# Optimization experiments

Measured on AMD Instinct MI355X. Metric: run time of the kernel, lower is better.

Reference implementation:

```python
import jax, jax.numpy as jnp
import numpy as np


def _l2norm(x, eps=1e-6):
    return x / jnp.sqrt(jnp.sum(x * x, axis=-1, keepdims=True) + eps)


def setup_inputs() -> dict:
    key = jax.random.key(0)
    k1, k2, k3, k4 = jax.random.split(key, 4)
    b, h, L, dk, dv = 2, 8, 4096, 128, 128
    q = jax.random.normal(k1, (b, h, L, dk), jnp.float32)
    k = jax.random.normal(k2, (b, h, L, dk), jnp.float32)
    v = jax.random.normal(k3, (b, h, L, dv), jnp.float32)
    beta = jax.random.uniform(k4, (b, h, L), jnp.float32)  # sigmoid(b_proj) in module -> (0,1)
    return {"q": q, "k": k, "v": v, "beta": beta, "chunk_size": 32}


def _delta_rule_chunkwise(q, k, v, beta, chunk_size):
    b, h, L, dk = q.shape
    dv = v.shape[-1]
    c = chunk_size
    pad = (-L) % c
    if pad:
        q = jnp.pad(q, ((0, 0), (0, 0), (0, pad), (0, 0)))
        k = jnp.pad(k, ((0, 0), (0, 0), (0, pad), (0, 0)))
        v = jnp.pad(v, ((0, 0), (0, 0), (0, pad), (0, 0)))
        beta = jnp.pad(beta, ((0, 0), (0, 0), (0, pad)))
    Lp = L + pad
    n = Lp // c

    q = _l2norm(q)
    k = _l2norm(k)
    v = v * beta[..., None]
    kb = k * beta[..., None]

    # (b,h,n,c,d)
    resh = lambda t: t.reshape(b, h, n, c, t.shape[-1])
    q, k, v, kb = resh(q), resh(k), resh(v), resh(kb)

    tri = jnp.triu(jnp.ones((c, c), bool), 0)        # upper incl diag
    tri_s = jnp.triu(jnp.ones((c, c), bool), 1)      # strict upper

    # forward substitution: inv = (I + strictly-lower(k_beta k^T))^{-1}-style recurrence
    inv = -jnp.einsum('bhncd,bhned->bhnce', kb, k)
    inv = jnp.where(tri, 0.0, inv)
    for i in range(1, c):  # fixed small chunk_size loop (c=32)
        upd = jnp.einsum('bhnk,bhnkj->bhnj', inv[..., i, :], inv[..., :, :i])
        inv = inv.at[..., i, :i].add(upd)
    inv = inv + jnp.eye(c, dtype=inv.dtype)

    u = inv @ v    # (b,h,n,c,dv)
    w = inv @ kb   # (b,h,n,c,dk)

    # chunk-recurrent state scan over the n blocks
    qs = jnp.moveaxis(q, 2, 0)
    ks = jnp.moveaxis(k, 2, 0)
    us = jnp.moveaxis(u, 2, 0)
    ws = jnp.moveaxis(w, 2, 0)
    S0 = jnp.zeros((b, h, dk, dv), q.dtype)

    def step(S, blk):
        q_i, k_i, u_i, w_i = blk
        attn = jnp.einsum('bhcd,bhed->bhce', q_i, k_i)
        attn = jnp.where(tri_s, 0.0, attn)                       # causal within chunk
        u_i = u_i - jnp.einsum('bhcd,bhde->bhce', w_i, S)
        o_i = jnp.einsum('bhcd,bhde->bhce', q_i, S) + jnp.einsum('bhce,bhed->bhcd', attn, u_i)
        S = S + jnp.einsum('bhcd,bhce->bhde', k_i, u_i)
        return S, o_i

    S, out = jax.lax.scan(step, S0, (qs, ks, us, ws))
    out = jnp.moveaxis(out, 0, 2).reshape(b, h, Lp, dv)[:, :, :L]
    return out, S


def reference(q, k, v, beta, chunk_size):
    return _delta_rule_chunkwise(q, k, v, beta, int(chunk_size))
```

## Files before the change

### kernel.cpp

```cpp
#include <hip/hip_runtime.h>
#include <cstddef>

#define BH   16
#define LSEQ 4096
#define DK   128
#define DV   128
#define C    32
#define NCH  128
#define DVB  16
#define NDVB 8
#define PP   136
#define PC   40
#define PS   136
#define AP   33

#define RECSZ 22528
#define OQ    0
#define OWH   4096
#define OWL   8192
#define OKTH  12288
#define OKTL  16384
#define OATH  20480
#define OATL  21504

typedef __attribute__((ext_vector_type(4))) float f32x4;
typedef __attribute__((ext_vector_type(8))) short short8;
typedef __attribute__((ext_vector_type(4))) short s16x4;

__device__ inline unsigned split_bf16(float x) {
    unsigned u = __builtin_bit_cast(unsigned, x);
    unsigned r = u + 0x7fffu + ((u >> 16) & 1u);
    unsigned h = r >> 16;
    float hf = __builtin_bit_cast(float, r & 0xffff0000u);
    float res = x - hf;
    unsigned u2 = __builtin_bit_cast(unsigned, res);
    unsigned r2 = u2 + 0x7fffu + ((u2 >> 16) & 1u);
    return (h << 16) | (r2 >> 16);
}
__device__ inline short hi_bf16(float x) {
    unsigned u = __builtin_bit_cast(unsigned, x);
    return (short)((u + 0x7fffu + ((u >> 16) & 1u)) >> 16);
}
__device__ inline short trunc_bf16(float x) {
    return (short)(__builtin_bit_cast(unsigned, x) >> 16);
}

__device__ inline short8 fld(const short* P, int row0, int pitch, int k0, int lane) {
    return *(const short8*)(P + (row0 + (lane & 15)) * pitch + k0 + ((lane >> 4) << 3));
}
__device__ inline short8 fldz128(const short* P, int row0, int ks, int lane) {
    int row = row0 + (lane & 15);
    int c = ks * 4 + (lane >> 4);
    return *(const short8*)(P + row * 128 + ((c ^ (row & 7)) << 3));
}
__device__ inline short8 fldz32(const short* P, int row0, int lane) {
    int row = row0 + (lane & 15);
    int c = lane >> 4;
    return *(const short8*)(P + row * 32 + ((c ^ (row & 3)) << 3));
}
__device__ inline f32x4 mf(short8 a, short8 b, f32x4 c) {
    return __builtin_amdgcn_mfma_f32_16x16x32_bf16(a, b, c, 0, 0, 0);
}
__device__ inline void build_ifrags(int lane, short8& Iev, short8& Iod) {
    int n = lane & 15, q = lane >> 4;
#pragma unroll
    for (int j = 0; j < 8; ++j) {
        Iev[j] = (q * 8 + j == n)      ? (short)0x3F80 : (short)0;
        Iod[j] = (q * 8 + j == n + 16) ? (short)0x3F80 : (short)0;
    }
}
__device__ inline void store8_z128(short* Pg, int row, int col0, s16x4 v) {
    int c = col0 >> 3;
    *(s16x4*)(Pg + row * 128 + ((c ^ (row & 7)) << 3) + (col0 & 7)) = v;
}
__device__ inline void store8_z32(short* Pg, int row, int col0, s16x4 v) {
    int c = col0 >> 3;
    *(s16x4*)(Pg + row * 32 + ((c ^ (row & 3)) << 3) + (col0 & 7)) = v;
}
__device__ inline void dma1k(const short* g, short* l, int lane) {
    __builtin_amdgcn_global_load_lds(
        (const __attribute__((address_space(1))) unsigned int*)(g + lane * 8),
        (__attribute__((address_space(3))) unsigned int*)l, 16, 0, 0);
}

__global__ __launch_bounds__(512) void k_prep(const float* __restrict__ Q,
                                              const float* __restrict__ K,
                                              const float* __restrict__ V,
                                              const float* __restrict__ Beta,
                                              short* __restrict__ RECg,
                                              float* __restrict__ Uws) {
    __shared__ short knh[C * PP], knl[C * PP], vh[C * PP], vl[C * PP], qh[C * PP];
    __shared__ short knTh[DK * PC], knTl[DK * PC], vTh[DK * PC], vTl[DK * PC];
    __shared__ short Th[C * PC], Tl[C * PC];
    __shared__ float A[C * AP];
    __shared__ float sbeta[C];

    const int t = threadIdx.x, lane = t & 63, wv = t >> 6;
    const int quad = (t >> 4) & 3, l15 = t & 15;
    const int g = blockIdx.x;
    const size_t base = (size_t)g * (C * DK);
    short* rec = RECg + (size_t)g * RECSZ;
    short8 Iev, Iod;
    build_ifrags(lane, Iev, Iod);

    if (t < C) sbeta[t] = Beta[(size_t)(g >> 7) * LSEQ + (size_t)(g & 127) * C + t];

    {
        const int sr = t >> 4, sc = (t & 15) * 8;
        f32x4 kk[2], vv[2], qq[2];
#pragma unroll
        for (int g4 = 0; g4 < 2; ++g4) {
            kk[g4] = *(const f32x4*)(K + base + 8 * t + 4 * g4);
            vv[g4] = *(const f32x4*)(V + base + 8 * t + 4 * g4);
            qq[g4] = *(const f32x4*)(Q + base + 8 * t + 4 * g4);
        }
        float ssk = 0.f, ssq = 0.f;
#pragma unroll
        for (int g4 = 0; g4 < 2; ++g4) {
#pragma unroll
            for (int e = 0; e < 4; ++e) {
                ssk += kk[g4][e] * kk[g4][e];
                ssq += qq[g4][e] * qq[g4][e];
            }
        }
        ssk += __shfl_xor(ssk, 1); ssk += __shfl_xor(ssk, 2);
        ssk += __shfl_xor(ssk, 4); ssk += __shfl_xor(ssk, 8);
        ssq += __shfl_xor(ssq, 1); ssq += __shfl_xor(ssq, 2);
        ssq += __shfl_xor(ssq, 4); ssq += __shfl_xor(ssq, 8);
        const float rk = rsqrtf(ssk + 1e-6f), rq = rsqrtf(ssq + 1e-6f);
        short8 h8, l8, q8;
#pragma unroll
        for (int e = 0; e < 8; ++e) {
            unsigned p = split_bf16(kk[e >> 2][e & 3] * rk);
            h8[e] = (short)(p >> 16); l8[e] = (short)(p & 0xffffu);
        }
        *(short8*)(knh + sr * PP + sc) = h8;
        *(short8*)(knl + sr * PP + sc) = l8;
#pragma unroll
        for (int e = 0; e < 8; ++e) {
            unsigned p = split_bf16(vv[e >> 2][e & 3]);
            h8[e] = (short)(p >> 16); l8[e] = (short)(p & 0xffffu);
        }
        *(short8*)(vh + sr * PP + sc) = h8;
        *(short8*)(vl + sr * PP + sc) = l8;
#pragma unroll
        for (int e = 0; e < 8; ++e) q8[e] = hi_bf16(qq[e >> 2][e & 3] * rq);
        *(short8*)(qh + sr * PP + sc) = q8;
        int c = sc >> 3;
        *(short8*)(rec + OQ + sr * 128 + ((c ^ (sr & 7)) << 3)) = q8;
    }
    __syncthreads();

    if (wv < 3) {
        const int a0 = (wv == 0) ? 0 : 16;
        const int b0 = (wv == 2) ? 16 : 0;
        f32x4 acc = {0.f, 0.f, 0.f, 0.f};
#pragma unroll
        for (int ks = 0; ks < 4; ++ks) {
            short8 ah = fld(knh, a0, PP, ks * 32, lane);
            short8 al = fld(knl, a0, PP, ks * 32, lane);
            short8 bh_ = fld(knh, b0, PP, ks * 32, lane);
            short8 bl_ = fld(knl, b0, PP, ks * 32, lane);
            acc = mf(ah, bh_, mf(ah, bl_, mf(al, bh_, acc)));
        }
#pragma unroll
        for (int r = 0; r < 4; ++r) {
            int row = a0 + quad * 4 + r, col = b0 + l15;
            A[row * AP + col] = (row > col) ? -sbeta[row] * acc[r] : 0.f;
        }
        f32x4 at = {0.f, 0.f, 0.f, 0.f};
#pragma unroll
        for (int ks = 0; ks < 4; ++ks) {
            short8 kh_ = fld(knh, b0, PP, ks * 32, lane);
            short8 kl_ = fld(knl, b0, PP, ks * 32, lane);
            short8 qf = fld(qh, a0, PP, ks * 32, lane);
            at = mf(kh_, qf, mf(kl_, qf, at));
        }
        s16x4 h4, l4;
#pragma unroll
        for (int r = 0; r < 4; ++r) {
            int cj = b0 + quad * 4 + r, ci = a0 + l15;
            float v = (cj <= ci) ? at[r] : 0.f;
            unsigned p = split_bf16(v);
            h4[r] = (short)(p >> 16); l4[r] = (short)(p & 0xffffu);
        }
        store8_z32(rec + OATH, a0 + l15, b0 + quad * 4, h4);
        store8_z32(rec + OATL, a0 + l15, b0 + quad * 4, l4);
    } else if (wv == 3) {
#pragma unroll
        for (int r = 0; r < 4; ++r) A[l15 * AP + 16 + quad * 4 + r] = 0.f;
        s16x4 z = {0, 0, 0, 0};
        store8_z32(rec + OATH, l15, 16 + quad * 4, z);
        store8_z32(rec + OATL, l15, 16 + quad * 4, z);
    }
    __syncthreads();

    auto tplane1 = [&](const short* src, short* dst, short* gdst, int c0) {
#pragma unroll
        for (int ks = 0; ks < 4; ++ks) {
            short8 fr = fld(src, c0, PP, ks * 32, lane);
            f32x4 z = {0.f, 0.f, 0.f, 0.f};
            f32x4 cA = mf(fr, Iev, z);
            f32x4 cB = mf(fr, Iod, z);
            s16x4 sA, sB;
#pragma unroll
            for (int r = 0; r < 4; ++r) { sA[r] = trunc_bf16(cA[r]); sB[r] = trunc_bf16(cB[r]); }
            *(s16x4*)(dst + (ks * 32 + l15) * PC + c0 + quad * 4) = sA;
            *(s16x4*)(dst + (ks * 32 + 16 + l15) * PC + c0 + quad * 4) = sB;
            if (gdst) {
                store8_z32(gdst, ks * 32 + l15, c0 + quad * 4, sA);
                store8_z32(gdst, ks * 32 + 16 + l15, c0 + quad * 4, sB);
            }
        }
    };
    if (wv == 0)      tplane1(knh, knTh, rec + OKTH, 0);
    else if (wv == 4) tplane1(knh, knTh, rec + OKTH, 16);
    else if (wv == 1) tplane1(knl, knTl, rec + OKTL, 0);
    else if (wv == 5) tplane1(knl, knTl, rec + OKTL, 16);
    else if (wv == 2) tplane1(vh, vTh, nullptr, 0);
    else if (wv == 6) tplane1(vh, vTh, nullptr, 16);
    else if (wv == 7) { tplane1(vl, vTl, nullptr, 0); tplane1(vl, vTl, nullptr, 16); }
    else if (lane < C) {
        const int j = lane;
        for (int i = 1; i < C; ++i) {
            float upd = 0.f;
            for (int kk2 = 1; kk2 < i; ++kk2) upd += A[i * AP + kk2] * A[kk2 * AP + j];
            if (j < i) A[i * AP + j] += upd;
        }
    }
    __syncthreads();

    if (t < 256) {
        int tr = t >> 3, tc = (t & 7) * 4;
        s16x4 h4, l4;
#pragma unroll
        for (int e = 0; e < 4; ++e) {
            int j = tc + e;
            float val = ((tr == j) ? 1.f : (tr > j ? A[tr * AP + j] : 0.f)) * sbeta[j];
            unsigned p = split_bf16(val);
            h4[e] = (short)(p >> 16); l4[e] = (short)(p & 0xffffu);
        }
        *(s16x4*)(Th + tr * PC + tc) = h4;
        *(s16x4*)(Tl + tr * PC + tc) = l4;
    }
    __syncthreads();

    {
        const int ci0 = (wv & 1) * 16;
        short8 bTh = fld(Th, ci0, PC, 0, lane);
        short8 bTl = fld(Tl, ci0, PC, 0, lane);
        if (wv < 4) {
            const int tb = (wv >> 1) * 4;
#pragma unroll
            for (int k = 0; k < 4; ++k) {
                int tt = tb + k;
                short8 ah = fld(vTh, tt * 16, PC, 0, lane);
                short8 al = fld(vTl, tt * 16, PC, 0, lane);
                f32x4 z = {0.f, 0.f, 0.f, 0.f};
                f32x4 acc = mf(ah, bTh, mf(ah, bTl, mf(al, bTh, z)));
                *(f32x4*)(Uws + (size_t)g * 4096 + (size_t)(ci0 + l15) * DK + tt * 16 + quad * 4) = acc;
            }
        } else {
            const int tb = ((wv - 4) >> 1) * 4;
#pragma unroll
            for (int k = 0; k < 4; ++k) {
                int tt = tb + k;
                short8 ah = fld(knTh, tt * 16, PC, 0, lane);
                short8 al = fld(knTl, tt * 16, PC, 0, lane);
                f32x4 z = {0.f, 0.f, 0.f, 0.f};
                f32x4 acc = mf(ah, bTh, mf(ah, bTl, mf(al, bTh, z)));
                s16x4 h4, l4;
#pragma unroll
                for (int r = 0; r < 4; ++r) {
                    unsigned p = split_bf16(acc[r]);
                    h4[r] = (short)(p >> 16); l4[r] = (short)(p & 0xffffu);
                }
                store8_z128(rec + OWH, ci0 + l15, tt * 16 + quad * 4, h4);
                store8_z128(rec + OWL, ci0 + l15, tt * 16 + quad * 4, l4);
            }
        }
    }
}

__global__ __launch_bounds__(512, 1) void k_scan(const short* __restrict__ RECg,
                                                 const float* __restrict__ Uws,
                                                 float* __restrict__ Out,
                                                 float* __restrict__ Sout) {
    __shared__ __attribute__((aligned(16))) short bALL[2][RECSZ];
    __shared__ short STh[DVB * PS], STl[DVB * PS];
    __shared__ short uTh[DVB * PC], uTl[DVB * PC];

    const int t = threadIdx.x, lane = t & 63, wv = t >> 6;
    const int quad = (t >> 4) & 3, l15 = t & 15;
    const int db = blockIdx.x >> 4, bhi = blockIdx.x & 15;
    const int vcol = db * DVB;
    const int r0 = (wv & 1) * 16;
    const int dk0 = wv * 16;
    const size_t gb = (size_t)bhi * NCH;

    f32x4 accS = {0.f, 0.f, 0.f, 0.f};
    float pu[4] = {0.f, 0.f, 0.f, 0.f};

    auto dma_chunk = [&](int cc, int s) {
        if (wv < 2) return;
        const short* src = RECg + (size_t)(gb + cc) * RECSZ;
        short* dst = bALL[s];
#pragma unroll
        for (int k = 0; k < 8; ++k) {
            int q = (wv - 2) + 6 * k;
            if (q < 44) dma1k(src + q * 512, dst + q * 512, lane);
        }
    };
    auto pref_u = [&](int cc) {
        if (wv < 2) {
            const size_t ub = (gb + cc) * 4096;
#pragma unroll
            for (int r = 0; r < 4; ++r)
                pu[r] = Uws[ub + (size_t)(r0 + quad * 4 + r) * DK + vcol + l15];
        }
    };

    for (int e = t; e < DVB * PS; e += 512) { STh[e] = 0; STl[e] = 0; }
    dma_chunk(0, 0);
    pref_u(0);
    __syncthreads();

    for (int cid = 0; cid < NCH; ++cid) {
        const int cur = cid & 1;
        const short* pC = bALL[cur];
        f32x4 oc = {0.f, 0.f, 0.f, 0.f};

        short8 kth = fldz32(pC + OKTH, dk0, lane);
        short8 ktl = fldz32(pC + OKTL, dk0, lane);
        short8 bah = {}, bal = {};

        if (wv >= 2) {
            if (cid + 1 < NCH) dma_chunk(cid + 1, cur ^ 1);
        } else {
            float p0 = pu[0], p1 = pu[1], p2 = pu[2], p3 = pu[3];
            if (cid + 1 < NCH) pref_u(cid + 1);

            f32x4 u0 = {-p0, -p1, -p2, -p3};
            f32x4 u1 = {0.f, 0.f, 0.f, 0.f}, u2 = {0.f, 0.f, 0.f, 0.f};
            f32x4 o1 = {0.f, 0.f, 0.f, 0.f};
#pragma unroll
            for (int ks = 0; ks < 4; ++ks) {
                short8 wh_ = fldz128(pC + OWH, r0, ks, lane);
                short8 wl_ = fldz128(pC + OWL, r0, ks, lane);
                short8 sh_ = fld(STh, 0, PS, ks * 32, lane);
                short8 sl_ = fld(STl, 0, PS, ks * 32, lane);
                short8 qf = fldz128(pC + OQ, r0, ks, lane);
                u0 = mf(wh_, sh_, u0);
                u1 = mf(wh_, sl_, u1);
                u2 = mf(wl_, sh_, u2);
                oc = mf(sh_, qf, oc);
                o1 = mf(sl_, qf, o1);
            }
            oc += o1;
            f32x4 us = u0 + u1 + u2;
            s16x4 h4, l4;
#pragma unroll
            for (int r = 0; r < 4; ++r) {
                unsigned p = split_bf16(-us[r]);
                h4[r] = (short)(p >> 16); l4[r] = (short)(p & 0xffffu);
            }
            *(s16x4*)(uTh + l15 * PC + r0 + quad * 4) = h4;
            *(s16x4*)(uTl + l15 * PC + r0 + quad * 4) = l4;
            bah = fldz32(pC + OATH, r0, lane);
            bal = fldz32(pC + OATL, r0, lane);
        }
        __syncthreads();

        short8 buh = fld(uTh, 0, PC, 0, lane);
        short8 bul = fld(uTl, 0, PC, 0, lane);
        if (wv < 2) {
            oc = mf(buh, bah, mf(buh, bal, mf(bul, bah, oc)));
            const size_t ob = ((size_t)bhi * LSEQ + (size_t)cid * C) * DK;
            *(f32x4*)(Out + ob + (size_t)(r0 + l15) * DK + vcol + quad * 4) = oc;
        }
        {
            f32x4 z = {0.f, 0.f, 0.f, 0.f};
            f32x4 tband = mf(kth, bul, mf(ktl, buh, z));
            accS = mf(kth, buh, accS);
            accS += tband;
            s16x4 h4, l4;
#pragma unroll
            for (int r = 0; r < 4; ++r) {
                unsigned p = split_bf16(accS[r]);
                h4[r] = (short)(p >> 16); l4[r] = (short)(p & 0xffffu);
            }
            *(s16x4*)(STh + l15 * PS + dk0 + quad * 4) = h4;
            *(s16x4*)(STl + l15 * PS + dk0 + quad * 4) = l4;
        }
        __syncthreads();
    }

#pragma unroll
    for (int r = 0; r < 4; ++r)
        Sout[(size_t)bhi * DK * DV + (size_t)(dk0 + quad * 4 + r) * DV + vcol + l15] = accS[r];
}

extern "C" void kernel_launch(void* const* d_in, const int* in_sizes, int n_in,
                              void* d_out, int out_size, void* d_ws, size_t ws_size,
                              hipStream_t stream) {
    const float* Q    = (const float*)d_in[0];
    const float* K    = (const float*)d_in[1];
    const float* V    = (const float*)d_in[2];
    const float* Beta = (const float*)d_in[3];

    float* Out  = (float*)d_out;
    float* Sout = Out + (size_t)BH * LSEQ * DV;

    short* RECg = (short*)d_ws;
    float* Uws  = (float*)(RECg + (size_t)BH * NCH * RECSZ);

    hipLaunchKernelGGL(k_prep, dim3(BH * NCH), dim3(512), 0, stream,
                       Q, K, V, Beta, RECg, Uws);
    hipLaunchKernelGGL(k_scan, dim3(BH * NDVB), dim3(512), 0, stream,
                       RECg, Uws, Out, Sout);
}
```

Baseline: 339.9 us.

## Compute u redundantly per wave to drop one block barrier per chunk

Every wave now computes the full 32-row u correction (S·W) itself and writes it to a private LDS slot. This removes the barrier that previously separated the u computation in two waves from the state update in all eight waves. The output computation moves to waves 2 and 3, and the DMA prefetch moves to the other six waves. The chunk loop is unrolled by two with separate named buffers and register prefetch arrays, so buffer indexing is static. The cost is redundant MFMA work, more LDS reads of W and S per wave, and higher register pressure.

Result: slower. 430.4 us (+26.6%).

```diff
diff --git a/kernel.cpp b/kernel.cpp
--- a/kernel.cpp
+++ b/kernel.cpp
@@ -286,77 +286,85 @@
                                                  const float* __restrict__ Uws,
                                                  float* __restrict__ Out,
                                                  float* __restrict__ Sout) {
-    __shared__ __attribute__((aligned(16))) short bALL[2][RECSZ];
+    __shared__ __attribute__((aligned(16))) short bufA[RECSZ];
+    __shared__ __attribute__((aligned(16))) short bufB[RECSZ];
     __shared__ short STh[DVB * PS], STl[DVB * PS];
-    __shared__ short uTh[DVB * PC], uTl[DVB * PC];
+    __shared__ short uSh[8][16 * PC], uSl[8][16 * PC];
 
     const int t = threadIdx.x, lane = t & 63, wv = t >> 6;
     const int quad = (t >> 4) & 3, l15 = t & 15;
     const int db = blockIdx.x >> 4, bhi = blockIdx.x & 15;
     const int vcol = db * DVB;
-    const int r0 = (wv & 1) * 16;
+    const int r02 = (wv & 1) * 16;
     const int dk0 = wv * 16;
     const size_t gb = (size_t)bhi * NCH;
+    const bool owv = (wv == 2 || wv == 3);
+    const int widx = (wv < 2) ? wv : wv - 2;
 
     f32x4 accS = {0.f, 0.f, 0.f, 0.f};
-    float pu[4] = {0.f, 0.f, 0.f, 0.f};
-
-    auto dma_chunk = [&](int cc, int s) {
-        if (wv < 2) return;
+    float puA[8], puB[8];
+#pragma unroll
+    for (int r = 0; r < 8; ++r) { puA[r] = 0.f; puB[r] = 0.f; }
+    short* const myUh = &uSh[wv][0];
+    short* const myUl = &uSl[wv][0];
+
+    auto dma_chunk = [&](int cc, short* dst) {
         const short* src = RECg + (size_t)(gb + cc) * RECSZ;
-        short* dst = bALL[s];
 #pragma unroll
         for (int k = 0; k < 8; ++k) {
-            int q = (wv - 2) + 6 * k;
+            int q = widx + 6 * k;
             if (q < 44) dma1k(src + q * 512, dst + q * 512, lane);
         }
     };
-    auto pref_u = [&](int cc) {
-        if (wv < 2) {
-            const size_t ub = (gb + cc) * 4096;
-#pragma unroll
-            for (int r = 0; r < 4; ++r)
-                pu[r] = Uws[ub + (size_t)(r0 + quad * 4 + r) * DK + vcol + l15];
+    auto pref_u = [&](int cc, float* p) {
+        const size_t ub = (gb + cc) * 4096;
+#pragma unroll
+        for (int r = 0; r < 4; ++r) {
+            p[r]     = Uws[ub + (size_t)(quad * 4 + r) * DK + vcol + l15];
+            p[4 + r] = Uws[ub + (size_t)(16 + quad * 4 + r) * DK + vcol + l15];
         }
     };
 
     for (int e = t; e < DVB * PS; e += 512) { STh[e] = 0; STl[e] = 0; }
-    dma_chunk(0, 0);
-    pref_u(0);
+    if (!owv) dma_chunk(0, bufA);
+    pref_u(0, puA);
     __syncthreads();
 
-    for (int cid = 0; cid < NCH; ++cid) {
-        const int cur = cid & 1;
-        const short* pC = bALL[cur];
-        f32x4 oc = {0.f, 0.f, 0.f, 0.f};
-
-        short8 kth = fldz32(pC + OKTH, dk0, lane);
-        short8 ktl = fldz32(pC + OKTL, dk0, lane);
-        short8 bah = {}, bal = {};
-
-        if (wv >= 2) {
-            if (cid + 1 < NCH) dma_chunk(cid + 1, cur ^ 1);
-        } else {
-            float p0 = pu[0], p1 = pu[1], p2 = pu[2], p3 = pu[3];
-            if (cid + 1 < NCH) pref_u(cid + 1);
-
-            f32x4 u0 = {-p0, -p1, -p2, -p3};
+    auto body = [&](int cid, const short* R, short* Wb, const float* puC, float* puN) {
+        short8 kth = fldz32(R + OKTH, dk0, lane);
+        short8 ktl = fldz32(R + OKTL, dk0, lane);
+        short8 Sh[4], Sl[4], WhA[4], WlA[4], WhB[4], WlB[4];
+#pragma unroll
+        for (int ks = 0; ks < 4; ++ks) {
+            Sh[ks]  = fld(STh, 0, PS, ks * 32, lane);
+            Sl[ks]  = fld(STl, 0, PS, ks * 32, lane);
+            WhA[ks] = fldz128(R + OWH, 0,  ks, lane);
+            WlA[ks] = fldz128(R + OWL, 0,  ks, lane);
+            WhB[ks] = fldz128(R + OWH, 16, ks, lane);
+            WlB[ks] = fldz128(R + OWL, 16, ks, lane);
+        }
+        short8 qf0 = {}, qf1 = {}, qf2 = {}, qf3 = {}, bah = {}, bal = {};
+        if (owv) {
+            qf0 = fldz128(R + OQ, r02, 0, lane);
+            qf1 = fldz128(R + OQ, r02, 1, lane);
+            qf2 = fldz128(R + OQ, r02, 2, lane);
+            qf3 = fldz128(R + OQ, r02, 3, lane);
+            bah = fldz32(R + OATH, r02, lane);
+            bal = fldz32(R + OATL, r02, lane);
+        }
+        if (cid + 1 < NCH) {
+            if (!owv) dma_chunk(cid + 1, Wb);
+            pref_u(cid + 1, puN);
+        }
+        {
+            f32x4 u0 = {-puC[0], -puC[1], -puC[2], -puC[3]};
             f32x4 u1 = {0.f, 0.f, 0.f, 0.f}, u2 = {0.f, 0.f, 0.f, 0.f};
-            f32x4 o1 = {0.f, 0.f, 0.f, 0.f};
 #pragma unroll
             for (int ks = 0; ks < 4; ++ks) {
-                short8 wh_ = fldz128(pC + OWH, r0, ks, lane);
-                short8 wl_ = fldz128(pC + OWL, r0, ks, lane);
-                short8 sh_ = fld(STh, 0, PS, ks * 32, lane);
-                short8 sl_ = fld(STl, 0, PS, ks * 32, lane);
-                short8 qf = fldz128(pC + OQ, r0, ks, lane);
-                u0 = mf(wh_, sh_, u0);
-                u1 = mf(wh_, sl_, u1);
-                u2 = mf(wl_, sh_, u2);
-                oc = mf(sh_, qf, oc);
-                o1 = mf(sl_, qf, o1);
-            }
-            oc += o1;
+                u0 = mf(WhA[ks], Sh[ks], u0);
+                u1 = mf(WhA[ks], Sl[ks], u1);
+                u2 = mf(WlA[ks], Sh[ks], u2);
+            }
             f32x4 us = u0 + u1 + u2;
             s16x4 h4, l4;
 #pragma unroll
@@ -364,25 +372,36 @@
                 unsigned p = split_bf16(-us[r]);
                 h4[r] = (short)(p >> 16); l4[r] = (short)(p & 0xffffu);
             }
-            *(s16x4*)(uTh + l15 * PC + r0 + quad * 4) = h4;
-            *(s16x4*)(uTl + l15 * PC + r0 + quad * 4) = l4;
-            bah = fldz32(pC + OATH, r0, lane);
-            bal = fldz32(pC + OATL, r0, lane);
-        }
-        __syncthreads();
-
-        short8 buh = fld(uTh, 0, PC, 0, lane);
-        short8 bul = fld(uTl, 0, PC, 0, lane);
-        if (wv < 2) {
-            oc = mf(buh, bah, mf(buh, bal, mf(bul, bah, oc)));
-            const size_t ob = ((size_t)bhi * LSEQ + (size_t)cid * C) * DK;
-            *(f32x4*)(Out + ob + (size_t)(r0 + l15) * DK + vcol + quad * 4) = oc;
-        }
+            *(s16x4*)(myUh + l15 * PC + quad * 4) = h4;
+            *(s16x4*)(myUl + l15 * PC + quad * 4) = l4;
+        }
+        {
+            f32x4 u0 = {-puC[4], -puC[5], -puC[6], -puC[7]};
+            f32x4 u1 = {0.f, 0.f, 0.f, 0.f}, u2 = {0.f, 0.f, 0.f, 0.f};
+#pragma unroll
+            for (int ks = 0; ks < 4; ++ks) {
+                u0 = mf(WhB[ks], Sh[ks], u0);
+                u1 = mf(WhB[ks], Sl[ks], u1);
+                u2 = mf(WlB[ks], Sh[ks], u2);
+            }
+            f32x4 us = u0 + u1 + u2;
+            s16x4 h4, l4;
+#pragma unroll
+            for (int r = 0; r < 4; ++r) {
+                unsigned p = split_bf16(-us[r]);
+                h4[r] = (short)(p >> 16); l4[r] = (short)(p & 0xffffu);
+            }
+            *(s16x4*)(myUh + l15 * PC + 16 + quad * 4) = h4;
+            *(s16x4*)(myUl + l15 * PC + 16 + quad * 4) = l4;
+        }
+        short8 buh = fld(myUh, 0, PC, 0, lane);
+        short8 bul = fld(myUl, 0, PC, 0, lane);
         {
             f32x4 z = {0.f, 0.f, 0.f, 0.f};
-            f32x4 tband = mf(kth, bul, mf(ktl, buh, z));
+            f32x4 ta = mf(ktl, buh, z);
+            f32x4 tb = mf(kth, bul, z);
             accS = mf(kth, buh, accS);
-            accS += tband;
+            accS += ta + tb;
             s16x4 h4, l4;
 #pragma unroll
             for (int r = 0; r < 4; ++r) {
@@ -392,7 +411,23 @@
             *(s16x4*)(STh + l15 * PS + dk0 + quad * 4) = h4;
             *(s16x4*)(STl + l15 * PS + dk0 + quad * 4) = l4;
         }
+        if (owv) {
+            f32x4 z = {0.f, 0.f, 0.f, 0.f};
+            f32x4 oa = mf(Sh[0], qf0, z), ob_ = mf(Sl[0], qf0, z);
+            f32x4 oc2 = mf(Sh[1], qf1, z), od = mf(Sl[1], qf1, z);
+            oa = mf(Sh[2], qf2, oa); ob_ = mf(Sl[2], qf2, ob_);
+            oc2 = mf(Sh[3], qf3, oc2); od = mf(Sl[3], qf3, od);
+            f32x4 osum = (oa + ob_) + (oc2 + od);
+            f32x4 oc = mf(buh, bah, mf(buh, bal, mf(bul, bah, osum)));
+            const size_t ob = ((size_t)bhi * LSEQ + (size_t)cid * C) * DK;
+            *(f32x4*)(Out + ob + (size_t)(r02 + l15) * DK + vcol + quad * 4) = oc;
+        }
         __syncthreads();
+    };
+
+    for (int cp = 0; cp < NCH / 2; ++cp) {
+        body(2 * cp,     bufA, bufB, puA, puB);
+        body(2 * cp + 1, bufB, bufA, puB, puA);
     }
 
 #pragma unroll
```
